# Performance work log

Measured on AMD Instinct MI355X. Metric: run time of the kernel, lower is better.

## Reference

```python
import jax, jax.numpy as jnp
import numpy as np

N_NODES = 50000
N_EDGES = 600000
D_FEAT = 128
HIDDEN = 128
N_STEPS = 4


def setup_inputs() -> dict:
    key = jax.random.key(0)
    ks = jax.random.split(key, 10)
    node = jax.random.normal(ks[0], (N_NODES, D_FEAT), dtype=jnp.float32)
    edges = jax.random.randint(ks[1], (2, N_EDGES), 0, N_NODES, dtype=jnp.int64)
    edges_attr = jax.random.uniform(ks[2], (N_EDGES,), dtype=jnp.float32)
    s = 1.0 / np.sqrt(HIDDEN)
    W1 = jax.random.normal(ks[3], (D_FEAT, HIDDEN), dtype=jnp.float32) * s
    b1 = jnp.zeros((HIDDEN,), dtype=jnp.float32)
    Ws = jax.random.normal(ks[4], (N_STEPS, HIDDEN, HIDDEN), dtype=jnp.float32) * s
    bs = jnp.zeros((N_STEPS, HIDDEN), dtype=jnp.float32)
    Wfc = jax.random.normal(ks[5], (HIDDEN, 2), dtype=jnp.float32) * s
    bfc = jnp.zeros((2,), dtype=jnp.float32)
    return {"node": node, "edges": edges, "edges_attr": edges_attr,
            "W1": W1, "b1": b1, "Ws": Ws, "bs": bs, "Wfc": Wfc, "bfc": bfc}


def _gcn_norm(edges, edges_attr, n_nodes):
    # PyG gcn_norm with add_self_loops=True (fill 1.0)
    loop = jnp.arange(n_nodes, dtype=edges.dtype)
    row = jnp.concatenate([edges[0], loop])  # source
    col = jnp.concatenate([edges[1], loop])  # target
    ew = jnp.concatenate([edges_attr, jnp.ones((n_nodes,), dtype=edges_attr.dtype)])
    deg = jax.ops.segment_sum(ew, col, num_segments=n_nodes)
    dinv = jnp.where(deg > 0, jax.lax.rsqrt(jnp.where(deg > 0, deg, 1.0)), 0.0)
    norm = dinv[row] * ew * dinv[col]  # [E+N]
    return row, col, norm


def _gcn_conv(x, row, col, norm, W, b, n_nodes):
    h = x @ W                               # [N, H]
    msg = h[row] * norm[:, None]            # gather + scale [E+N, H]
    agg = jax.ops.segment_sum(msg, col, num_segments=n_nodes)  # scatter-add
    return agg + b


def reference(node, edges, edges_attr, W1, b1, Ws, bs, Wfc, bfc):
    n_nodes = node.shape[0]
    row, col, norm = _gcn_norm(edges, edges_attr, n_nodes)
    x = jax.nn.relu(_gcn_conv(node, row, col, norm, W1, b1, n_nodes))
    for i in range(Ws.shape[0]):
        x_res = x
        x = _gcn_conv(x, row, col, norm, Ws[i], bs[i], n_nodes)
        x = jax.nn.relu(x + x_res)  # residual=True
    x = x @ Wfc + bfc               # [N, 2]
    return jnp.mean(x, axis=0, keepdims=True)  # global_mean_pool(batch=None) -> [1, 2]
```

## Files before the change

### kernel.cpp

```cpp
#include <hip/hip_runtime.h>

#define N_NODES 50000
#define N_EDGES 600000
#define HID 128
#define NCOPY 8

typedef __attribute__((ext_vector_type(8))) short bf16x8;
typedef __attribute__((ext_vector_type(8))) unsigned short u16x8;
typedef __attribute__((ext_vector_type(4))) float f32x4;
typedef __attribute__((ext_vector_type(2))) float f32x2;

__device__ __forceinline__ float bf2f(unsigned short u) {
    return __uint_as_float(((unsigned int)u) << 16);
}
__device__ __forceinline__ unsigned short f2bf(float f) {
    unsigned int u = __float_as_uint(f);
    u = (u + 0x7FFFu + ((u >> 16) & 1u)) >> 16;
    return (unsigned short)u;
}

__device__ __forceinline__ unsigned char fp8enc_hw(float f) {
    return (unsigned char)(__builtin_amdgcn_cvt_pk_fp8_f32(f, f, 0, false) & 0xff);
}


__global__ __launch_bounds__(256) void init_k(unsigned long long* degcnt8, float* cs, int total) {
    int i = blockIdx.x * 256 + threadIdx.x;
    if (i < total) degcnt8[i] = (i < N_NODES) ? (1ull << 32) : 0ull;
    if (i < HID) cs[i] = 0.0f;
}

__global__ __launch_bounds__(256) void edge_deg_k(const int* __restrict__ edges,
                                                  const float* __restrict__ attr,
                                                  unsigned long long* degcnt8,
                                                  int* __restrict__ rank) {
    int e = blockIdx.x * 256 + threadIdx.x;
    int copy = blockIdx.x & (NCOPY - 1);
    if (e < N_EDGES) {
        int c = edges[N_EDGES + e];
        unsigned long long enc = (1ull << 43) +
            (unsigned long long)llrintf(attr[e] * 4294967296.0f);
        unsigned long long old = atomicAdd(&degcnt8[(size_t)copy * N_NODES + c], enc);
        rank[e] = (int)(old >> 43);
    }
}

__global__ __launch_bounds__(256) void scan1_k(const unsigned long long* __restrict__ degcnt8,
                                               int* offs, int* bsum, float* dinv,
                                               int* __restrict__ cbase, int n) {
    __shared__ int s[256];
    int tid = threadIdx.x;
    int i = blockIdx.x * 256 + tid;
    int v = 0;
    if (i < n) {
        unsigned long long attrsum = 0;
        int running = 0;
        #pragma unroll
        for (int c = 0; c < NCOPY; ++c) {
            unsigned long long dc = degcnt8[(size_t)c * n + i];
            cbase[i * NCOPY + c] = running;
            running += (int)(dc >> 43);
            attrsum += dc & ((1ull << 43) - 1);
        }
        v = running;
        float deg = (float)attrsum * (1.0f / 4294967296.0f);
        dinv[i] = rsqrtf(deg);
    }
    s[tid] = v; __syncthreads();
    for (int d = 1; d < 256; d <<= 1) {
        int t = (tid >= d) ? s[tid - d] : 0;
        __syncthreads();
        s[tid] += t;
        __syncthreads();
    }
    if (i < n) offs[i] = s[tid] - v;
    if (tid == 255) bsum[blockIdx.x] = s[255];
}

__global__ __launch_bounds__(256) void scan3_k(int* offs, const int* __restrict__ bsum,
                                               int* cbase, int n, int nb) {
    __shared__ int s[256];
    int tid = threadIdx.x;
    int bv = (tid < nb) ? bsum[tid] : 0;
    s[tid] = bv; __syncthreads();
    for (int d = 1; d < 256; d <<= 1) {
        int t = (tid >= d) ? s[tid - d] : 0;
        __syncthreads();
        s[tid] += t;
        __syncthreads();
    }
    int b = blockIdx.x;
    int pbase = s[b] - bsum[b];
    int i = b * 256 + tid;
    if (i < n) {
        int v = offs[i] + pbase;
        offs[i] = v;
        #pragma unroll
        for (int c = 0; c < NCOPY; ++c) cbase[i * NCOPY + c] += v;
    }
}

__global__ __launch_bounds__(256) void fill_k(const int* __restrict__ edges,
                                              const float* __restrict__ attr,
                                              const float* __restrict__ dinv,
                                              const int* __restrict__ cbase,
                                              const int* __restrict__ rank,
                                              int2* __restrict__ epk) {
    int e = blockIdx.x * 256 + threadIdx.x;
    int copy = blockIdx.x & (NCOPY - 1);
    if (e < N_EDGES) {
        int r = edges[e];
        int c = edges[N_EDGES + e];
        float w = dinv[r] * attr[e] * dinv[c];
        epk[cbase[c * NCOPY + copy] + rank[e]] = make_int2(r, __float_as_int(w));
    }
}

__global__ __launch_bounds__(256) void prep_w_k(const float* __restrict__ W1,
                                                const float* __restrict__ Ws,
                                                unsigned short* __restrict__ Wt_hi,
                                                unsigned short* __restrict__ Wt_lo) {
    int i = blockIdx.x * 256 + threadIdx.x;
    if (i >= 5 * 16384) return;
    int l = i >> 14;
    int r = i & 16383;
    int n = r >> 7;
    int k = r & 127;
    const float* src = (l == 0) ? W1 : (Ws + (size_t)(l - 1) * 16384);
    float w = src[k * 128 + n];
    unsigned short hi = f2bf(w);
    unsigned short lo = f2bf(w - bf2f(hi));
    Wt_hi[i] = hi;
    Wt_lo[i] = lo;
}


template <bool FP32A>
__global__ __launch_bounds__(256) void mfma_gemm_k(const void* __restrict__ Av,
                                                   const unsigned short* __restrict__ Bh,
                                                   const unsigned short* __restrict__ Bl,
                                                   unsigned char* __restrict__ H, int nrows) {
    int wid  = threadIdx.x >> 6;
    int lane = threadIdx.x & 63;
    int row0 = blockIdx.x * 256 + wid * 64;
    int rl = lane & 15;
    int kg = lane >> 4;

    bf16x8 af[4][4];
    #pragma unroll
    for (int rt = 0; rt < 4; ++rt) {
        int row = row0 + rt * 16 + rl;
        int ar  = row < nrows ? row : nrows - 1;
        #pragma unroll
        for (int kt = 0; kt < 4; ++kt) {
            if (FP32A) {
                const float* Af = (const float*)Av;
                float4 v0 = *(const float4*)(Af + (size_t)ar * HID + kt * 32 + kg * 8);
                float4 v1 = *(const float4*)(Af + (size_t)ar * HID + kt * 32 + kg * 8 + 4);
                bf16x8 t;
                t[0] = (short)f2bf(v0.x); t[1] = (short)f2bf(v0.y);
                t[2] = (short)f2bf(v0.z); t[3] = (short)f2bf(v0.w);
                t[4] = (short)f2bf(v1.x); t[5] = (short)f2bf(v1.y);
                t[6] = (short)f2bf(v1.z); t[7] = (short)f2bf(v1.w);
                af[rt][kt] = t;
            } else {
                const unsigned short* Ab = (const unsigned short*)Av;
                af[rt][kt] = *(const bf16x8*)(Ab + (size_t)ar * HID + kt * 32 + kg * 8);
            }
        }
    }

    f32x4 acc[4][8];
    #pragma unroll
    for (int rt = 0; rt < 4; ++rt)
        #pragma unroll
        for (int nt = 0; nt < 8; ++nt) acc[rt][nt] = (f32x4){0.f, 0.f, 0.f, 0.f};

    #pragma unroll
    for (int nt = 0; nt < 8; ++nt) {
        #pragma unroll
        for (int kt = 0; kt < 4; ++kt) {
            size_t boff = (size_t)(nt * 16 + rl) * HID + kt * 32 + kg * 8;
            bf16x8 bh = *(const bf16x8*)(Bh + boff);
            bf16x8 bl = *(const bf16x8*)(Bl + boff);
            #pragma unroll
            for (int rt = 0; rt < 4; ++rt) {
                acc[rt][nt] = __builtin_amdgcn_mfma_f32_16x16x32_bf16(af[rt][kt], bh, acc[rt][nt], 0, 0, 0);
                acc[rt][nt] = __builtin_amdgcn_mfma_f32_16x16x32_bf16(af[rt][kt], bl, acc[rt][nt], 0, 0, 0);
            }
        }
    }

    #pragma unroll
    for (int rt = 0; rt < 4; ++rt) {
        #pragma unroll
        for (int nt = 0; nt < 8; ++nt) {
            #pragma unroll
            for (int r = 0; r < 4; ++r) {
                int orow = row0 + rt * 16 + kg * 4 + r;
                if (orow < nrows)
                    H[(size_t)orow * HID + nt * 16 + rl] = fp8enc_hw(acc[rt][nt][r]);
            }
        }
    }
}


__device__ __forceinline__ void dec_fma8_pk(uint2 q, float wt, f32x2* a) {
    f32x2 w2 = {wt, wt};
    a[0] += __builtin_amdgcn_cvt_pk_f32_fp8((int)q.x, false) * w2;
    a[1] += __builtin_amdgcn_cvt_pk_f32_fp8((int)q.x, true)  * w2;
    a[2] += __builtin_amdgcn_cvt_pk_f32_fp8((int)q.y, false) * w2;
    a[3] += __builtin_amdgcn_cvt_pk_f32_fp8((int)q.y, true)  * w2;
}

__global__ __launch_bounds__(256) void aggregate_k(const unsigned char* __restrict__ h,
                                                   const int* __restrict__ offs,
                                                   const int2* __restrict__ epk,
                                                   const float* __restrict__ dinv,
                                                   const float* __restrict__ bias,
                                                   const unsigned short* __restrict__ xprev,
                                                   unsigned short* __restrict__ xout, int n) {
    int wave = (blockIdx.x * 256 + threadIdx.x) >> 6;
    int lane = threadIdx.x & 63;
    int g  = lane >> 4;
    int ci = (lane & 15) * 8;
    int w = wave * 4 + g;

    f32x2 a[4];
    #pragma unroll
    for (int j = 0; j < 4; ++j) a[j] = (f32x2){0.f, 0.f};

    int e0 = 0, e1 = 0;
    if (w < n) {
        e0 = offs[w];
        e1 = (w + 1 < n) ? offs[w + 1] : N_EDGES;
    }

    for (int e = e0; e < e1; e += 8) {
        int2 pk[8];
        uint2 q[8];
        #pragma unroll
        for (int u = 0; u < 8; ++u)
            if (e + u < e1) pk[u] = epk[e + u];
        #pragma unroll
        for (int u = 0; u < 8; ++u)
            if (e + u < e1)
                q[u] = *(const uint2*)(h + (size_t)pk[u].x * HID + ci);
        #pragma unroll
        for (int u = 0; u < 8; ++u)
            if (e + u < e1)
                dec_fma8_pk(q[u], __int_as_float(pk[u].y), a);
    }

    if (w < n) {
        float di = dinv[w];
        uint2 qw = *(const uint2*)(h + (size_t)w * HID + ci);
        dec_fma8_pk(qw, di * di, a);
        float av[8] = {a[0][0], a[0][1], a[1][0], a[1][1],
                       a[2][0], a[2][1], a[3][0], a[3][1]};
        float4 b0 = *(const float4*)(bias + ci);
        float4 b1 = *(const float4*)(bias + ci + 4);
        av[0] += b0.x; av[1] += b0.y; av[2] += b0.z; av[3] += b0.w;
        av[4] += b1.x; av[5] += b1.y; av[6] += b1.z; av[7] += b1.w;
        if (xprev) {
            u16x8 xp = *(const u16x8*)(xprev + (size_t)w * HID + ci);
            #pragma unroll
            for (int j = 0; j < 8; ++j) av[j] += bf2f(xp[j]);
        }
        u16x8 o;
        #pragma unroll
        for (int j = 0; j < 8; ++j) o[j] = f2bf(fmaxf(av[j], 0.f));
        *(u16x8*)(xout + (size_t)w * HID + ci) = o;
    }
}


__global__ __launch_bounds__(128) void colsum_k(const unsigned short* __restrict__ x, float* cs, int n) {
    int col = threadIdx.x;
    float acc = 0.f;
    for (int r = blockIdx.x; r < n; r += gridDim.x)
        acc += bf2f(x[(size_t)r * HID + col]);
    atomicAdd(&cs[col], acc);
}

__global__ __launch_bounds__(128) void final_k(const float* __restrict__ cs,
                                               const float* __restrict__ Wfc,
                                               const float* __restrict__ bfc,
                                               float* __restrict__ out) {
    __shared__ float s0[128], s1[128];
    int k = threadIdx.x;
    float c = cs[k];
    s0[k] = c * Wfc[k * 2 + 0];
    s1[k] = c * Wfc[k * 2 + 1];
    __syncthreads();
    for (int d = 64; d > 0; d >>= 1) {
        if (k < d) { s0[k] += s0[k + d]; s1[k] += s1[k + d]; }
        __syncthreads();
    }
    if (k == 0) {
        out[0] = s0[0] / (float)N_NODES + bfc[0];
        out[1] = s1[0] / (float)N_NODES + bfc[1];
    }
}


extern "C" void kernel_launch(void* const* d_in, const int* in_sizes, int n_in,
                              void* d_out, int out_size, void* d_ws, size_t ws_size,
                              hipStream_t stream) {
    const float* node  = (const float*)d_in[0];
    const int*   edges = (const int*)d_in[1];
    const float* attr  = (const float*)d_in[2];
    const float* W1    = (const float*)d_in[3];
    const float* b1    = (const float*)d_in[4];
    const float* Ws    = (const float*)d_in[5];
    const float* bs    = (const float*)d_in[6];
    const float* Wfc   = (const float*)d_in[7];
    const float* bfc   = (const float*)d_in[8];
    float* out = (float*)d_out;

    char* ws = (char*)d_ws;
    const size_t BN = (size_t)N_NODES * HID * 2;
    unsigned char*  h8     = (unsigned char*)(ws);
    unsigned short* xa_bf  = (unsigned short*)(ws + BN);
    unsigned short* xb_bf  = (unsigned short*)(ws + 2 * BN);
    char* p = ws + 3 * BN;
    unsigned long long* degcnt8 = (unsigned long long*)p; p += (size_t)NCOPY * N_NODES * 8;
    float* dinv  = (float*)p;            p += N_NODES * 4;
    int*   offs  = (int*)p;              p += N_NODES * 4;
    int*   cbase = (int*)p;              p += (size_t)N_NODES * NCOPY * 4;
    int*   rank  = (int*)p;              p += (size_t)N_EDGES * 4;
    int*   bsum  = (int*)p;              p += 1024;
    int2*  epk   = (int2*)p;             p += (size_t)N_EDGES * 8;
    float* cs    = (float*)p;            p += 512;
    unsigned short* wt_hi = (unsigned short*)p;  p += 5 * 16384 * 2;
    unsigned short* wt_lo = (unsigned short*)p;  p += 5 * 16384 * 2;

    const int NB_N  = (N_NODES + 255) / 256;
    const int NB_N8 = (NCOPY * N_NODES + 255) / 256;
    const int NB_E  = (N_EDGES + 255) / 256;

    hipLaunchKernelGGL(init_k,    dim3(NB_N8), dim3(256), 0, stream, degcnt8, cs, NCOPY * N_NODES);
    hipLaunchKernelGGL(edge_deg_k,dim3(NB_E),  dim3(256), 0, stream, edges, attr, degcnt8, rank);
    hipLaunchKernelGGL(scan1_k,   dim3(NB_N),  dim3(256), 0, stream, degcnt8, offs, bsum, dinv, cbase, N_NODES);
    hipLaunchKernelGGL(scan3_k,   dim3(NB_N),  dim3(256), 0, stream, offs, bsum, cbase, N_NODES, NB_N);
    hipLaunchKernelGGL(fill_k,    dim3(NB_E),  dim3(256), 0, stream, edges, attr, dinv, cbase, rank, epk);
    hipLaunchKernelGGL(prep_w_k,  dim3(320),   dim3(256), 0, stream, W1, Ws, wt_hi, wt_lo);

    const int GB = (N_NODES + 255) / 256;
    const int AB = (N_NODES + 15) / 16;

    hipLaunchKernelGGL((mfma_gemm_k<true>), dim3(GB), dim3(256), 0, stream,
                       (const void*)node, wt_hi, wt_lo, h8, N_NODES);
    hipLaunchKernelGGL(aggregate_k, dim3(AB), dim3(256), 0, stream, h8, offs, epk, dinv,
                       b1, (const unsigned short*)nullptr, xa_bf, N_NODES);

    unsigned short* xc = xa_bf;
    unsigned short* xn = xb_bf;
    for (int i = 0; i < 4; ++i) {
        hipLaunchKernelGGL((mfma_gemm_k<false>), dim3(GB), dim3(256), 0, stream,
                           (const void*)xc, wt_hi + (size_t)(i + 1) * 16384,
                           wt_lo + (size_t)(i + 1) * 16384, h8, N_NODES);
        hipLaunchKernelGGL(aggregate_k, dim3(AB), dim3(256), 0, stream, h8, offs, epk, dinv,
                           bs + (size_t)i * HID, xc, xn, N_NODES);
        unsigned short* t = xc; xc = xn; xn = t;
    }

    hipLaunchKernelGGL(colsum_k, dim3(512), dim3(128), 0, stream, xc, cs, N_NODES);
    hipLaunchKernelGGL(final_k,  dim3(1),   dim3(128), 0, stream, cs, Wfc, bfc, out);
}
```

Baseline: 287.1 us.

## Split aggregate columns into halves across XCD-interleaved blocks, add nontemporal loads

Each aggregate block now covers one 64-column half for 32 nodes instead of all 128 columns for 16 nodes. Block IDs are remapped so the two halves of a node group land on different groups of 4 consecutive block IDs, which likely map to different XCDs, so each XCD's L2 holds only half the feature columns. Edge metadata, the residual input and the output are marked nontemporal to avoid polluting the cache. The cost is that edge lists are read twice, once per half, and each gather is shorter, only 64 columns wide.

```diff
diff --git a/kernel.cpp b/kernel.cpp
--- a/kernel.cpp
+++ b/kernel.cpp
@@ -9,6 +9,8 @@
 typedef __attribute__((ext_vector_type(8))) unsigned short u16x8;
 typedef __attribute__((ext_vector_type(4))) float f32x4;
 typedef __attribute__((ext_vector_type(2))) float f32x2;
+typedef __attribute__((ext_vector_type(2))) int i32x2;
+typedef __attribute__((ext_vector_type(2))) unsigned int u32x2;
 
 __device__ __forceinline__ float bf2f(unsigned short u) {
     return __uint_as_float(((unsigned int)u) << 16);
@@ -221,39 +223,41 @@
                                                    const float* __restrict__ bias,
                                                    const unsigned short* __restrict__ xprev,
                                                    unsigned short* __restrict__ xout, int n) {
-    int wave = (blockIdx.x * 256 + threadIdx.x) >> 6;
+    int bid = blockIdx.x;
+    int half  = (bid & 7) >> 2;
+    int islot = (bid >> 3) * 4 + (bid & 3);
     int lane = threadIdx.x & 63;
-    int g  = lane >> 4;
-    int ci = (lane & 15) * 8;
-    int w = wave * 4 + g;
+    int wave = threadIdx.x >> 6;
+    int g  = lane >> 3;
+    int ci = half * 64 + (lane & 7) * 8;
+    int w = islot * 32 + wave * 8 + g;
+
+    if (w >= n) return;
 
     f32x2 a[4];
     #pragma unroll
     for (int j = 0; j < 4; ++j) a[j] = (f32x2){0.f, 0.f};
 
-    int e0 = 0, e1 = 0;
-    if (w < n) {
-        e0 = offs[w];
-        e1 = (w + 1 < n) ? offs[w + 1] : N_EDGES;
-    }
+    int e0 = offs[w];
+    int e1 = (w + 1 < n) ? offs[w + 1] : N_EDGES;
 
     for (int e = e0; e < e1; e += 8) {
-        int2 pk[8];
+        i32x2 pk[8];
         uint2 q[8];
         #pragma unroll
         for (int u = 0; u < 8; ++u)
-            if (e + u < e1) pk[u] = epk[e + u];
+            if (e + u < e1) pk[u] = __builtin_nontemporal_load((const i32x2*)&epk[e + u]);
         #pragma unroll
         for (int u = 0; u < 8; ++u)
             if (e + u < e1)
-                q[u] = *(const uint2*)(h + (size_t)pk[u].x * HID + ci);
+                q[u] = *(const uint2*)(h + (size_t)pk[u][0] * HID + ci);
         #pragma unroll
         for (int u = 0; u < 8; ++u)
             if (e + u < e1)
-                dec_fma8_pk(q[u], __int_as_float(pk[u].y), a);
-    }
-
-    if (w < n) {
+                dec_fma8_pk(q[u], __int_as_float(pk[u][1]), a);
+    }
+
+    {
         float di = dinv[w];
         uint2 qw = *(const uint2*)(h + (size_t)w * HID + ci);
         dec_fma8_pk(qw, di * di, a);
@@ -264,14 +268,14 @@
         av[0] += b0.x; av[1] += b0.y; av[2] += b0.z; av[3] += b0.w;
         av[4] += b1.x; av[5] += b1.y; av[6] += b1.z; av[7] += b1.w;
         if (xprev) {
-            u16x8 xp = *(const u16x8*)(xprev + (size_t)w * HID + ci);
+            u16x8 xp = __builtin_nontemporal_load((const u16x8*)(xprev + (size_t)w * HID + ci));
             #pragma unroll
             for (int j = 0; j < 8; ++j) av[j] += bf2f(xp[j]);
         }
         u16x8 o;
         #pragma unroll
         for (int j = 0; j < 8; ++j) o[j] = f2bf(fmaxf(av[j], 0.f));
-        *(u16x8*)(xout + (size_t)w * HID + ci) = o;
+        __builtin_nontemporal_store(o, (u16x8*)(xout + (size_t)w * HID + ci));
     }
 }
 
@@ -348,7 +352,7 @@
     hipLaunchKernelGGL(prep_w_k,  dim3(320),   dim3(256), 0, stream, W1, Ws, wt_hi, wt_lo);
 
     const int GB = (N_NODES + 255) / 256;
-    const int AB = (N_NODES + 15) / 16;
+    const int AB = 392 * 8;
 
     hipLaunchKernelGGL((mfma_gemm_k<true>), dim3(GB), dim3(256), 0, stream,
                        (const void*)node, wt_hi, wt_lo, h8, N_NODES);
```

Measured after the change: 421.8 us. +46.9%, slower.
